# Kernel tuning notes

Measured on AMD Instinct MI355X. Metric: run time of the kernel, lower is better.

Reference implementation:

```python
import jax, jax.numpy as jnp
import numpy as np

N_NODES = 100000
N_EDGES = 1600000
D = 128


def setup_inputs() -> dict:
    key = jax.random.key(0)
    k1, k2, k3, k4 = jax.random.split(key, 4)
    x = jax.random.normal(k1, (N_NODES, D), dtype=jnp.float32)
    edge_index = jax.random.randint(k2, (2, N_EDGES), 0, N_NODES, dtype=jnp.int32)
    # torch.nn.Linear(nfeat, nclass): weight [out, in], bias [out]
    W = jax.random.normal(k3, (D, D), dtype=jnp.float32) * (1.0 / np.sqrt(D))
    b = jax.random.normal(k4, (D,), dtype=jnp.float32) * 0.01
    return {"x": x, "edge_index": edge_index, "W": W, "b": b}


def reference(x, edge_index, W, b):
    n = x.shape[0]
    # gcn_norm: add self-loops, edge_weight = 1
    loop = jnp.arange(n, dtype=edge_index.dtype)
    row = jnp.concatenate([edge_index[0], loop])  # source
    col = jnp.concatenate([edge_index[1], loop])  # target
    deg = jax.ops.segment_sum(jnp.ones_like(col, dtype=x.dtype), col, num_segments=n)
    dinv = jnp.where(deg > 0, deg ** -0.5, 0.0)
    norm = dinv[row] * dinv[col]  # [E+N]
    # K=1 propagate: out[col] += norm * x[row]
    agg = jax.ops.segment_sum(x[row] * norm[:, None], col, num_segments=n)
    # linear (y = agg @ W^T + b), then relu + residual
    h = agg @ W.T + b
    return x + jax.nn.relu(h)
```

## Files before the change

kernel.cpp:

```cpp
#include <hip/hip_runtime.h>

#define NN 100000
#define NE 1600000
#define DD 128
#define NBLK 98
#define NBUK 782
#define NB_AC 256
#define CHUNK 6250
#define SCAN_N (NBUK * NB_AC)
#define NB_SCAN 196

typedef __attribute__((ext_vector_type(8))) short bf16x8;
typedef __attribute__((ext_vector_type(4))) float f32x4;
typedef __attribute__((ext_vector_type(2))) float f32x2;

__device__ __forceinline__ float bf2f(unsigned short u) {
    return __uint_as_float(((unsigned)u) << 16);
}
__device__ __forceinline__ unsigned short f2bf(float f) {
    unsigned u = __float_as_uint(f);
    u += 0x7FFFu + ((u >> 16) & 1u);
    return (unsigned short)(u >> 16);
}

__global__ __launch_bounds__(1024) void k_hist(const int* __restrict__ col,
                                               unsigned* __restrict__ part) {
    __shared__ unsigned hist[NBUK];
    int t = threadIdx.x, blk = blockIdx.x;
    for (int i = t; i < NBUK; i += 1024) hist[i] = 0;
    __syncthreads();
    int beg = blk * CHUNK, end = beg + CHUNK;
    for (int e = beg + t; e < end; e += 1024)
        atomicAdd(&hist[col[e] >> 7], 1u);
    __syncthreads();
    for (int i = t; i < NBUK; i += 1024)
        part[(size_t)i * NB_AC + blk] = hist[i];
}

__global__ __launch_bounds__(1024) void k_bsum(const unsigned* __restrict__ part,
                                               unsigned* __restrict__ sb) {
    __shared__ unsigned red[1024];
    int t = threadIdx.x;
    int i = blockIdx.x * 1024 + t;
    red[t] = i < SCAN_N ? part[i] : 0;
    __syncthreads();
    for (int off = 512; off > 0; off >>= 1) {
        if (t < off) red[t] += red[t + off];
        __syncthreads();
    }
    if (t == 0) sb[blockIdx.x] = red[0];
}

__global__ __launch_bounds__(1024) void k_scanpart(const unsigned* __restrict__ part,
                                                   const unsigned* __restrict__ sb,
                                                   unsigned* __restrict__ off) {
    __shared__ unsigned s2[256];
    __shared__ unsigned s[1024];
    int t = threadIdx.x;
    if (t < 256) s2[t] = (t < NB_SCAN) ? sb[t] : 0;
    __syncthreads();
    for (int o = 1; o < 256; o <<= 1) {
        unsigned v = 0;
        if (t < 256 && t >= o) v = s2[t - o];
        __syncthreads();
        if (t < 256) s2[t] += v;
        __syncthreads();
    }
    unsigned boff = blockIdx.x == 0 ? 0 : s2[blockIdx.x - 1];
    int i = blockIdx.x * 1024 + t;
    unsigned v = i < SCAN_N ? part[i] : 0;
    s[t] = v;
    __syncthreads();
    for (int o = 1; o < 1024; o <<= 1) {
        unsigned u = t >= o ? s[t - o] : 0;
        __syncthreads();
        s[t] += u;
        __syncthreads();
    }
    if (i < SCAN_N) off[i] = boff + s[t] - v;
}

__global__ __launch_bounds__(1024) void k_scatter_pk(const int* __restrict__ row,
                                                     const int* __restrict__ col,
                                                     const unsigned* __restrict__ off,
                                                     unsigned* __restrict__ packed) {
    __shared__ unsigned cur[NBUK];
    int t = threadIdx.x, blk = blockIdx.x;
    for (int i = t; i < NBUK; i += 1024) cur[i] = off[(size_t)i * NB_AC + blk];
    __syncthreads();
    int beg = blk * CHUNK, end = beg + CHUNK;
    for (int e = beg + t; e < end; e += 1024) {
        int c = col[e];
        unsigned pos = atomicAdd(&cur[c >> 7], 1u);
        packed[pos] = ((unsigned)(c & 127) << 17) | (unsigned)row[e];
    }
}

__global__ __launch_bounds__(256) void k_bucket_csr(const unsigned* __restrict__ off,
                                                    const unsigned* __restrict__ packed,
                                                    float* __restrict__ dinv,
                                                    int* __restrict__ rowptr,
                                                    int* __restrict__ esrc) {
    __shared__ unsigned deg[128], pre[128], tmp[128];
    int t = threadIdx.x;
    int buk = blockIdx.x;
    unsigned bstart = off[(size_t)buk * NB_AC];
    unsigned bend = (buk == NBUK - 1) ? (unsigned)NE : off[(size_t)(buk + 1) * NB_AC];
    if (t < 128) deg[t] = 0;
    __syncthreads();
    for (unsigned e = bstart + t; e < bend; e += 256)
        atomicAdd(&deg[packed[e] >> 17], 1u);
    __syncthreads();
    if (t < 128) tmp[t] = deg[t];
    __syncthreads();
    for (int o = 1; o < 128; o <<= 1) {
        unsigned v = 0;
        if (t < 128 && t >= o) v = tmp[t - o];
        __syncthreads();
        if (t < 128) tmp[t] += v;
        __syncthreads();
    }
    if (t < 128) {
        pre[t] = tmp[t] - deg[t];
        int n = buk * 128 + t;
        if (n < NN) {
            dinv[n] = 1.0f / sqrtf((float)(deg[t] + 1));
            rowptr[n] = (int)(bstart + pre[t]);
        }
    }
    if (buk == NBUK - 1 && t == 0) rowptr[NN] = NE;
    __syncthreads();
    if (t < 128) deg[t] = pre[t];
    __syncthreads();
    for (unsigned e = bstart + t; e < bend; e += 256) {
        unsigned p = packed[e];
        unsigned pos = atomicAdd(&deg[p >> 17], 1u);
        esrc[bstart + pos] = (int)(p & 0x1FFFFu);
    }
}

__global__ void k_wb(const float* __restrict__ W, unsigned short* __restrict__ wbs) {
    int unit = blockIdx.x * 256 + threadIdx.x;
    int row = unit >> 4;
    int c0 = (unit & 15) * 8;
    float4 v0 = *(const float4*)(W + row * DD + c0);
    float4 v1 = *(const float4*)(W + row * DD + c0 + 4);
    bf16x8 h;
    h[0] = (short)f2bf(v0.x); h[1] = (short)f2bf(v0.y);
    h[2] = (short)f2bf(v0.z); h[3] = (short)f2bf(v0.w);
    h[4] = (short)f2bf(v1.x); h[5] = (short)f2bf(v1.y);
    h[6] = (short)f2bf(v1.z); h[7] = (short)f2bf(v1.w);
    int byte = (row * 256 + c0 * 2) ^ ((row & 7) << 4);
    *(bf16x8*)((char*)wbs + byte) = h;
}

__global__ __launch_bounds__(256) void k_ygemm(const float* __restrict__ x,
                                               const unsigned short* __restrict__ wbs,
                                               const float* __restrict__ dinv,
                                               unsigned char* __restrict__ yb8) {
    __shared__ unsigned short wb[DD * DD];
    int t = threadIdx.x;
#pragma unroll
    for (int i = 0; i < 8; ++i)
        ((float4*)wb)[t + 256 * i] = ((const float4*)wbs)[t + 256 * i];
    __syncthreads();

    int wave = t >> 6;
    int lane = t & 63;
    int lrow = lane & 15;
    int kg = lane >> 4;

    int arow = blockIdx.x * 64 + wave * 16 + lrow;
    int arc = arow < NN ? arow : NN - 1;
    bf16x8 afrag[4];
#pragma unroll
    for (int ks = 0; ks < 4; ++ks) {
        const float* src = x + (size_t)arc * DD + ks * 32 + kg * 8;
        float4 v0 = *(const float4*)src;
        float4 v1 = *(const float4*)(src + 4);
        bf16x8 h;
        h[0] = (short)f2bf(v0.x); h[1] = (short)f2bf(v0.y);
        h[2] = (short)f2bf(v0.z); h[3] = (short)f2bf(v0.w);
        h[4] = (short)f2bf(v1.x); h[5] = (short)f2bf(v1.y);
        h[6] = (short)f2bf(v1.z); h[7] = (short)f2bf(v1.w);
        afrag[ks] = h;
    }

    f32x4 acc[8];
#pragma unroll
    for (int ct = 0; ct < 8; ++ct) acc[ct] = (f32x4)(0.f);

#pragma unroll
    for (int ct = 0; ct < 8; ++ct) {
        int wrow = ct * 16 + lrow;
#pragma unroll
        for (int ks = 0; ks < 4; ++ks) {
            int byte = (wrow * 256 + ks * 64 + kg * 16) ^ ((wrow & 7) << 4);
            bf16x8 bfrag = *(const bf16x8*)((char*)wb + byte);
            acc[ct] = __builtin_amdgcn_mfma_f32_16x16x32_bf16(afrag[ks], bfrag, acc[ct], 0, 0, 0);
        }
    }

#pragma unroll
    for (int j = 0; j < 4; ++j) {
        int m = blockIdx.x * 64 + wave * 16 + kg * 4 + j;
        if (m < NN) {
            float s = dinv[m];
            unsigned w0 = 0, w1 = 0;
            w0 = __builtin_amdgcn_cvt_pk_fp8_f32(s * acc[0][j], s * acc[1][j], w0, false);
            w0 = __builtin_amdgcn_cvt_pk_fp8_f32(s * acc[2][j], s * acc[3][j], w0, true);
            w1 = __builtin_amdgcn_cvt_pk_fp8_f32(s * acc[4][j], s * acc[5][j], w1, false);
            w1 = __builtin_amdgcn_cvt_pk_fp8_f32(s * acc[6][j], s * acc[7][j], w1, true);
            uint2 o; o.x = w0; o.y = w1;
            *(uint2*)(yb8 + (size_t)m * DD + lrow * 8) = o;
        }
    }
}

__global__ __launch_bounds__(256) void k_gather_fp8(const int* __restrict__ rowptr,
                                                    const int* __restrict__ esrc,
                                                    const unsigned char* __restrict__ yb8,
                                                    const float* __restrict__ x,
                                                    const float* __restrict__ dinv,
                                                    const float* __restrict__ bias,
                                                    float* __restrict__ out) {
    int t = threadIdx.x;
    int gl = t & 31;
    int node = blockIdx.x * 8 + (t >> 5);
    if (node >= NN) return;
    int beg = rowptr[node];
    int end = rowptr[node + 1];
    float dc = dinv[node];

    unsigned su = *(const unsigned*)(yb8 + (size_t)node * DD + gl * 4);
    f32x2 a01 = __builtin_amdgcn_cvt_pk_f32_fp8(su, false);
    f32x2 a23 = __builtin_amdgcn_cvt_pk_f32_fp8(su, true);

    int e = beg;
    for (; e + 7 < end; e += 8) {
        unsigned uu[8];
#pragma unroll
        for (int u = 0; u < 8; ++u) {
            int r = esrc[e + u];
            uu[u] = *(const unsigned*)(yb8 + (size_t)r * DD + gl * 4);
        }
#pragma unroll
        for (int u = 0; u < 8; ++u) {
            a01 += __builtin_amdgcn_cvt_pk_f32_fp8(uu[u], false);
            a23 += __builtin_amdgcn_cvt_pk_f32_fp8(uu[u], true);
        }
    }
    for (; e < end; ++e) {
        int r = esrc[e];
        unsigned u = *(const unsigned*)(yb8 + (size_t)r * DD + gl * 4);
        a01 += __builtin_amdgcn_cvt_pk_f32_fp8(u, false);
        a23 += __builtin_amdgcn_cvt_pk_f32_fp8(u, true);
    }

    float vals[4] = {a01.x, a01.y, a23.x, a23.y};
    int q = gl >> 1;
    int c0 = (gl & 1) * 4;
#pragma unroll
    for (int i = 0; i < 4; ++i) {
        int n = (c0 + i) * 16 + q;
        float h = dc * vals[i] + bias[n];
        out[(size_t)node * DD + n] = x[(size_t)node * DD + n] + fmaxf(h, 0.f);
    }
}

__global__ void k_count(const int* __restrict__ col, int* __restrict__ deg) {
    int i = blockIdx.x * blockDim.x + threadIdx.x;
    if (i < NE) atomicAdd(&deg[col[i]], 1);
}
__global__ __launch_bounds__(1024) void k_blocksum_dinv(const int* __restrict__ deg,
                                                        int* __restrict__ bsum,
                                                        float* __restrict__ dinv) {
    __shared__ int red[1024];
    int t = threadIdx.x;
    int i = blockIdx.x * 1024 + t;
    int d = i < NN ? deg[i] : 0;
    if (i < NN) dinv[i] = 1.0f / sqrtf((float)(d + 1));
    red[t] = d;
    __syncthreads();
    for (int off = 512; off > 0; off >>= 1) {
        if (t < off) red[t] += red[t + off];
        __syncthreads();
    }
    if (t == 0) bsum[blockIdx.x] = red[0];
}
__global__ void k_scanbsum(const int* __restrict__ bsum, int* __restrict__ boff) {
    __shared__ int s[128];
    int t = threadIdx.x;
    s[t] = t < NBLK ? bsum[t] : 0;
    __syncthreads();
    for (int off = 1; off < 128; off <<= 1) {
        int v = t >= off ? s[t - off] : 0;
        __syncthreads();
        s[t] += v;
        __syncthreads();
    }
    if (t < NBLK) boff[t] = (t == 0) ? 0 : s[t - 1];
}
__global__ __launch_bounds__(1024) void k_scanwrite(const int* __restrict__ deg,
                                                    const int* __restrict__ boff,
                                                    int* __restrict__ rowptr) {
    __shared__ int s[1024];
    int t = threadIdx.x;
    int i = blockIdx.x * 1024 + t;
    int v = i < NN ? deg[i] : 0;
    s[t] = v;
    __syncthreads();
    for (int off = 1; off < 1024; off <<= 1) {
        int u = t >= off ? s[t - off] : 0;
        __syncthreads();
        s[t] += u;
        __syncthreads();
    }
    if (i < NN) rowptr[i] = boff[blockIdx.x] + s[t] - v;
    if (i == 0) rowptr[NN] = NE;
}
__global__ void k_fill(const int* __restrict__ row, const int* __restrict__ col,
                       const int* __restrict__ rowptr, int* __restrict__ cnt,
                       int* __restrict__ esrc) {
    int i = blockIdx.x * blockDim.x + threadIdx.x;
    if (i < NE) {
        int c = col[i];
        int pos = rowptr[c] + atomicAdd(&cnt[c], 1);
        esrc[pos] = row[i];
    }
}
__global__ __launch_bounds__(256) void k_gather(const int* __restrict__ rowptr,
                                                const int* __restrict__ esrc,
                                                const float* __restrict__ x,
                                                const float* __restrict__ dinv,
                                                float* __restrict__ agg) {
    int t = threadIdx.x;
    int lane = t & 31;
    int node = blockIdx.x * 8 + (t >> 5);
    if (node >= NN) return;
    int beg = rowptr[node];
    int end = rowptr[node + 1];
    float dc = dinv[node];
    float4 xv = ((const float4*)(x + (size_t)node * DD))[lane];
    float4 acc;
    acc.x = dc * xv.x; acc.y = dc * xv.y; acc.z = dc * xv.z; acc.w = dc * xv.w;
    int e = beg;
    for (; e + 1 < end; e += 2) {
        int r0 = esrc[e];
        int r1 = esrc[e + 1];
        float s0 = dinv[r0];
        float s1 = dinv[r1];
        float4 v0 = ((const float4*)(x + (size_t)r0 * DD))[lane];
        float4 v1 = ((const float4*)(x + (size_t)r1 * DD))[lane];
        acc.x += s0 * v0.x + s1 * v1.x;
        acc.y += s0 * v0.y + s1 * v1.y;
        acc.z += s0 * v0.z + s1 * v1.z;
        acc.w += s0 * v0.w + s1 * v1.w;
    }
    if (e < end) {
        int r = esrc[e];
        float s = dinv[r];
        float4 v = ((const float4*)(x + (size_t)r * DD))[lane];
        acc.x += s * v.x; acc.y += s * v.y; acc.z += s * v.z; acc.w += s * v.w;
    }
    acc.x *= dc; acc.y *= dc; acc.z *= dc; acc.w *= dc;
    ((float4*)(agg + (size_t)node * DD))[lane] = acc;
}
__global__ void k_transpose_w(const float* __restrict__ W, float* __restrict__ Wt) {
    int c = blockIdx.x;
    int k = threadIdx.x;
    Wt[k * DD + c] = W[c * DD + k];
}
__global__ __launch_bounds__(256) void k_gemm(const float* __restrict__ x,
                                              const float* __restrict__ Wt,
                                              const float* __restrict__ bias,
                                              float* __restrict__ out) {
    __shared__ float wt[DD * DD];
    int t = threadIdx.x;
    for (int i = t; i < DD * DD / 4; i += 256)
        ((float4*)wt)[i] = ((const float4*)Wt)[i];
    __syncthreads();

    int grp = t >> 5;
    int c4  = (t & 31) * 4;
    int rbase = blockIdx.x * 64 + grp * 8;

    float acc[8][4];
#pragma unroll
    for (int i = 0; i < 8; i++)
#pragma unroll
        for (int j = 0; j < 4; j++) acc[i][j] = 0.0f;

    for (int k = 0; k < DD; k += 4) {
        float4 w0 = *(const float4*)&wt[(k + 0) * DD + c4];
        float4 w1 = *(const float4*)&wt[(k + 1) * DD + c4];
        float4 w2 = *(const float4*)&wt[(k + 2) * DD + c4];
        float4 w3 = *(const float4*)&wt[(k + 3) * DD + c4];
#pragma unroll
        for (int i = 0; i < 8; i++) {
            int rr = rbase + i;
            rr = rr < NN ? rr : NN - 1;
            float4 a = *(const float4*)&out[(size_t)rr * DD + k];
            acc[i][0] += a.x * w0.x + a.y * w1.x + a.z * w2.x + a.w * w3.x;
            acc[i][1] += a.x * w0.y + a.y * w1.y + a.z * w2.y + a.w * w3.y;
            acc[i][2] += a.x * w0.z + a.y * w1.z + a.z * w2.z + a.w * w3.z;
            acc[i][3] += a.x * w0.w + a.y * w1.w + a.z * w2.w + a.w * w3.w;
        }
    }

    float4 bv = *(const float4*)&bias[c4];
#pragma unroll
    for (int i = 0; i < 8; i++) {
        int r = rbase + i;
        if (r < NN) {
            float4 xv = *(const float4*)&x[(size_t)r * DD + c4];
            float4 o;
            o.x = xv.x + fmaxf(acc[i][0] + bv.x, 0.0f);
            o.y = xv.y + fmaxf(acc[i][1] + bv.y, 0.0f);
            o.z = xv.z + fmaxf(acc[i][2] + bv.z, 0.0f);
            o.w = xv.w + fmaxf(acc[i][3] + bv.w, 0.0f);
            *(float4*)&out[(size_t)r * DD + c4] = o;
        }
    }
}

extern "C" void kernel_launch(void* const* d_in, const int* in_sizes, int n_in,
                              void* d_out, int out_size, void* d_ws, size_t ws_size,
                              hipStream_t stream) {
    const float* x   = (const float*)d_in[0];
    const int*   ei  = (const int*)d_in[1];
    const float* W   = (const float*)d_in[2];
    const float* b   = (const float*)d_in[3];
    const int* row = ei;
    const int* col = ei + NE;

    float* out = (float*)d_out;

    char* ws = (char*)d_ws;
    unsigned* part   = (unsigned*)ws;
    unsigned* off    = (unsigned*)(ws + 800768);
    unsigned* sb     = (unsigned*)(ws + 1601536);
    float*    dinv   = (float*)(ws + 1602352);
    int*      rowptr = (int*)(ws + 2002352);
    unsigned* packed = (unsigned*)(ws + 2402368);
    unsigned short* wbs = (unsigned short*)(ws + 8802368);
    float*    Wt     = (float*)(ws + 8802368);
    int*      esrc   = (int*)(ws + 8867904);
    unsigned char* yb8 = (unsigned char*)(ws + 15267904);

    bool big_ws = ws_size >= 28100000;

    if (big_ws) {
        k_hist<<<NB_AC, 1024, 0, stream>>>(col, part);
        k_bsum<<<NB_SCAN, 1024, 0, stream>>>(part, sb);
        k_scanpart<<<NB_SCAN, 1024, 0, stream>>>(part, sb, off);
        k_scatter_pk<<<NB_AC, 1024, 0, stream>>>(row, col, off, packed);
        k_bucket_csr<<<NBUK, 256, 0, stream>>>(off, packed, dinv, rowptr, esrc);
        k_wb<<<8, 256, 0, stream>>>(W, wbs);
        k_ygemm<<<(NN + 63) / 64, 256, 0, stream>>>(x, wbs, dinv, yb8);
        k_gather_fp8<<<(NN + 7) / 8, 256, 0, stream>>>(rowptr, esrc, yb8, x, dinv, b, out);
    } else {
        int* cnt  = (int*)ws;
        int* bsum = (int*)(ws + 1601536);
        int* boff = (int*)(ws + 400000);
        hipMemsetAsync(cnt, 0, NN * sizeof(int), stream);
        k_count<<<(NE + 255) / 256, 256, 0, stream>>>(col, cnt);
        k_blocksum_dinv<<<NBLK, 1024, 0, stream>>>(cnt, bsum, dinv);
        k_scanbsum<<<1, 128, 0, stream>>>(bsum, boff);
        k_scanwrite<<<NBLK, 1024, 0, stream>>>(cnt, boff, rowptr);
        hipMemsetAsync(cnt, 0, NN * sizeof(int), stream);
        k_fill<<<(NE + 255) / 256, 256, 0, stream>>>(row, col, rowptr, cnt, esrc);
        k_gather<<<(NN + 7) / 8, 256, 0, stream>>>(rowptr, esrc, x, dinv, out);
        k_transpose_w<<<DD, DD, 0, stream>>>(W, Wt);
        k_gemm<<<(NN + 63) / 64, 256, 0, stream>>>(x, Wt, b, out);
    }
}
```

Baseline: 124.4 us.

## Fuse bucket CSR build with fp8 GEMM and move source dinv scaling into gather

Merges the bucket-CSR kernel, the W bf16 conversion kernel and the y GEMM into one launch, with blocks split by index between CSR work and GEMM work. To remove the GEMM's dependency on dinv, the source-side normalisation moves into the gather, which now loads dinv[r] per edge and scales each fp8 row. Each GEMM block converts W to bf16 in shared memory itself, and the gather uses nontemporal loads and stores for x and out. The cost is an extra dinv load per edge plus redundant W conversion in every GEMM block, and the fp8 values are now quantised before the dinv scaling, which may change accuracy.

```diff
diff --git a/kernel.cpp b/kernel.cpp
--- a/kernel.cpp
+++ b/kernel.cpp
@@ -9,6 +9,7 @@
 #define CHUNK 6250
 #define SCAN_N (NBUK * NB_AC)
 #define NB_SCAN 196
+#define NB_YG ((NN + 63) / 64)
 
 typedef __attribute__((ext_vector_type(8))) short bf16x8;
 typedef __attribute__((ext_vector_type(4))) float f32x4;
@@ -96,123 +97,120 @@
     }
 }
 
-__global__ __launch_bounds__(256) void k_bucket_csr(const unsigned* __restrict__ off,
-                                                    const unsigned* __restrict__ packed,
-                                                    float* __restrict__ dinv,
-                                                    int* __restrict__ rowptr,
-                                                    int* __restrict__ esrc) {
+__global__ __launch_bounds__(256) void k_finalize(const unsigned* __restrict__ off,
+                                                  const unsigned* __restrict__ packed,
+                                                  float* __restrict__ dinv,
+                                                  int* __restrict__ rowptr,
+                                                  int* __restrict__ esrc,
+                                                  const float* __restrict__ x,
+                                                  const float* __restrict__ W,
+                                                  unsigned char* __restrict__ yb8) {
+    __shared__ unsigned short wb[DD * DD];
     __shared__ unsigned deg[128], pre[128], tmp[128];
     int t = threadIdx.x;
-    int buk = blockIdx.x;
-    unsigned bstart = off[(size_t)buk * NB_AC];
-    unsigned bend = (buk == NBUK - 1) ? (unsigned)NE : off[(size_t)(buk + 1) * NB_AC];
-    if (t < 128) deg[t] = 0;
-    __syncthreads();
-    for (unsigned e = bstart + t; e < bend; e += 256)
-        atomicAdd(&deg[packed[e] >> 17], 1u);
-    __syncthreads();
-    if (t < 128) tmp[t] = deg[t];
-    __syncthreads();
-    for (int o = 1; o < 128; o <<= 1) {
-        unsigned v = 0;
-        if (t < 128 && t >= o) v = tmp[t - o];
-        __syncthreads();
-        if (t < 128) tmp[t] += v;
-        __syncthreads();
-    }
-    if (t < 128) {
-        pre[t] = tmp[t] - deg[t];
-        int n = buk * 128 + t;
-        if (n < NN) {
-            dinv[n] = 1.0f / sqrtf((float)(deg[t] + 1));
-            rowptr[n] = (int)(bstart + pre[t]);
-        }
-    }
-    if (buk == NBUK - 1 && t == 0) rowptr[NN] = NE;
-    __syncthreads();
-    if (t < 128) deg[t] = pre[t];
-    __syncthreads();
-    for (unsigned e = bstart + t; e < bend; e += 256) {
-        unsigned p = packed[e];
-        unsigned pos = atomicAdd(&deg[p >> 17], 1u);
-        esrc[bstart + pos] = (int)(p & 0x1FFFFu);
-    }
-}
-
-__global__ void k_wb(const float* __restrict__ W, unsigned short* __restrict__ wbs) {
-    int unit = blockIdx.x * 256 + threadIdx.x;
-    int row = unit >> 4;
-    int c0 = (unit & 15) * 8;
-    float4 v0 = *(const float4*)(W + row * DD + c0);
-    float4 v1 = *(const float4*)(W + row * DD + c0 + 4);
-    bf16x8 h;
-    h[0] = (short)f2bf(v0.x); h[1] = (short)f2bf(v0.y);
-    h[2] = (short)f2bf(v0.z); h[3] = (short)f2bf(v0.w);
-    h[4] = (short)f2bf(v1.x); h[5] = (short)f2bf(v1.y);
-    h[6] = (short)f2bf(v1.z); h[7] = (short)f2bf(v1.w);
-    int byte = (row * 256 + c0 * 2) ^ ((row & 7) << 4);
-    *(bf16x8*)((char*)wbs + byte) = h;
-}
-
-__global__ __launch_bounds__(256) void k_ygemm(const float* __restrict__ x,
-                                               const unsigned short* __restrict__ wbs,
-                                               const float* __restrict__ dinv,
-                                               unsigned char* __restrict__ yb8) {
-    __shared__ unsigned short wb[DD * DD];
-    int t = threadIdx.x;
-#pragma unroll
-    for (int i = 0; i < 8; ++i)
-        ((float4*)wb)[t + 256 * i] = ((const float4*)wbs)[t + 256 * i];
-    __syncthreads();
-
-    int wave = t >> 6;
-    int lane = t & 63;
-    int lrow = lane & 15;
-    int kg = lane >> 4;
-
-    int arow = blockIdx.x * 64 + wave * 16 + lrow;
-    int arc = arow < NN ? arow : NN - 1;
-    bf16x8 afrag[4];
-#pragma unroll
-    for (int ks = 0; ks < 4; ++ks) {
-        const float* src = x + (size_t)arc * DD + ks * 32 + kg * 8;
-        float4 v0 = *(const float4*)src;
-        float4 v1 = *(const float4*)(src + 4);
-        bf16x8 h;
-        h[0] = (short)f2bf(v0.x); h[1] = (short)f2bf(v0.y);
-        h[2] = (short)f2bf(v0.z); h[3] = (short)f2bf(v0.w);
-        h[4] = (short)f2bf(v1.x); h[5] = (short)f2bf(v1.y);
-        h[6] = (short)f2bf(v1.z); h[7] = (short)f2bf(v1.w);
-        afrag[ks] = h;
-    }
-
-    f32x4 acc[8];
-#pragma unroll
-    for (int ct = 0; ct < 8; ++ct) acc[ct] = (f32x4)(0.f);
-
-#pragma unroll
-    for (int ct = 0; ct < 8; ++ct) {
-        int wrow = ct * 16 + lrow;
+
+    if (blockIdx.x < NBUK) {
+        int buk = blockIdx.x;
+        unsigned bstart = off[(size_t)buk * NB_AC];
+        unsigned bend = (buk == NBUK - 1) ? (unsigned)NE : off[(size_t)(buk + 1) * NB_AC];
+        if (t < 128) deg[t] = 0;
+        __syncthreads();
+        for (unsigned e = bstart + t; e < bend; e += 256)
+            atomicAdd(&deg[packed[e] >> 17], 1u);
+        __syncthreads();
+        if (t < 128) tmp[t] = deg[t];
+        __syncthreads();
+        for (int o = 1; o < 128; o <<= 1) {
+            unsigned v = 0;
+            if (t < 128 && t >= o) v = tmp[t - o];
+            __syncthreads();
+            if (t < 128) tmp[t] += v;
+            __syncthreads();
+        }
+        if (t < 128) {
+            pre[t] = tmp[t] - deg[t];
+            int n = buk * 128 + t;
+            if (n < NN) {
+                dinv[n] = 1.0f / sqrtf((float)(deg[t] + 1));
+                rowptr[n] = (int)(bstart + pre[t]);
+            }
+        }
+        if (buk == NBUK - 1 && t == 0) rowptr[NN] = NE;
+        __syncthreads();
+        if (t < 128) deg[t] = pre[t];
+        __syncthreads();
+        for (unsigned e = bstart + t; e < bend; e += 256) {
+            unsigned p = packed[e];
+            unsigned pos = atomicAdd(&deg[p >> 17], 1u);
+            esrc[bstart + pos] = (int)(p & 0x1FFFFu);
+        }
+    } else {
+        int blk = blockIdx.x - NBUK;
+#pragma unroll
+        for (int it = 0; it < 8; ++it) {
+            int unit = t + 256 * it;
+            int wrow = unit >> 4;
+            int c0 = (unit & 15) * 8;
+            float4 v0 = *(const float4*)(W + wrow * DD + c0);
+            float4 v1 = *(const float4*)(W + wrow * DD + c0 + 4);
+            bf16x8 h;
+            h[0] = (short)f2bf(v0.x); h[1] = (short)f2bf(v0.y);
+            h[2] = (short)f2bf(v0.z); h[3] = (short)f2bf(v0.w);
+            h[4] = (short)f2bf(v1.x); h[5] = (short)f2bf(v1.y);
+            h[6] = (short)f2bf(v1.z); h[7] = (short)f2bf(v1.w);
+            int byte = (wrow * 256 + c0 * 2) ^ ((wrow & 7) << 4);
+            *(bf16x8*)((char*)wb + byte) = h;
+        }
+        __syncthreads();
+
+        int wave = t >> 6;
+        int lane = t & 63;
+        int lrow = lane & 15;
+        int kg = lane >> 4;
+
+        int arow = blk * 64 + wave * 16 + lrow;
+        int arc = arow < NN ? arow : NN - 1;
+        bf16x8 afrag[4];
 #pragma unroll
         for (int ks = 0; ks < 4; ++ks) {
-            int byte = (wrow * 256 + ks * 64 + kg * 16) ^ ((wrow & 7) << 4);
-            bf16x8 bfrag = *(const bf16x8*)((char*)wb + byte);
-            acc[ct] = __builtin_amdgcn_mfma_f32_16x16x32_bf16(afrag[ks], bfrag, acc[ct], 0, 0, 0);
-        }
-    }
-
-#pragma unroll
-    for (int j = 0; j < 4; ++j) {
-        int m = blockIdx.x * 64 + wave * 16 + kg * 4 + j;
-        if (m < NN) {
-            float s = dinv[m];
-            unsigned w0 = 0, w1 = 0;
-            w0 = __builtin_amdgcn_cvt_pk_fp8_f32(s * acc[0][j], s * acc[1][j], w0, false);
-            w0 = __builtin_amdgcn_cvt_pk_fp8_f32(s * acc[2][j], s * acc[3][j], w0, true);
-            w1 = __builtin_amdgcn_cvt_pk_fp8_f32(s * acc[4][j], s * acc[5][j], w1, false);
-            w1 = __builtin_amdgcn_cvt_pk_fp8_f32(s * acc[6][j], s * acc[7][j], w1, true);
-            uint2 o; o.x = w0; o.y = w1;
-            *(uint2*)(yb8 + (size_t)m * DD + lrow * 8) = o;
+            const float* src = x + (size_t)arc * DD + ks * 32 + kg * 8;
+            float4 v0 = *(const float4*)src;
+            float4 v1 = *(const float4*)(src + 4);
+            bf16x8 h;
+            h[0] = (short)f2bf(v0.x); h[1] = (short)f2bf(v0.y);
+            h[2] = (short)f2bf(v0.z); h[3] = (short)f2bf(v0.w);
+            h[4] = (short)f2bf(v1.x); h[5] = (short)f2bf(v1.y);
+            h[6] = (short)f2bf(v1.z); h[7] = (short)f2bf(v1.w);
+            afrag[ks] = h;
+        }
+
+        f32x4 acc[8];
+#pragma unroll
+        for (int ct = 0; ct < 8; ++ct) acc[ct] = (f32x4)(0.f);
+
+#pragma unroll
+        for (int ct = 0; ct < 8; ++ct) {
+            int wrow = ct * 16 + lrow;
+#pragma unroll
+            for (int ks = 0; ks < 4; ++ks) {
+                int byte = (wrow * 256 + ks * 64 + kg * 16) ^ ((wrow & 7) << 4);
+                bf16x8 bfrag = *(const bf16x8*)((char*)wb + byte);
+                acc[ct] = __builtin_amdgcn_mfma_f32_16x16x32_bf16(afrag[ks], bfrag, acc[ct], 0, 0, 0);
+            }
+        }
+
+#pragma unroll
+        for (int j = 0; j < 4; ++j) {
+            int m = blk * 64 + wave * 16 + kg * 4 + j;
+            if (m < NN) {
+                unsigned w0 = 0, w1 = 0;
+                w0 = __builtin_amdgcn_cvt_pk_fp8_f32(acc[0][j], acc[1][j], w0, false);
+                w0 = __builtin_amdgcn_cvt_pk_fp8_f32(acc[2][j], acc[3][j], w0, true);
+                w1 = __builtin_amdgcn_cvt_pk_fp8_f32(acc[4][j], acc[5][j], w1, false);
+                w1 = __builtin_amdgcn_cvt_pk_fp8_f32(acc[6][j], acc[7][j], w1, true);
+                uint2 o; o.x = w0; o.y = w1;
+                *(uint2*)(yb8 + (size_t)m * DD + lrow * 8) = o;
+            }
         }
     }
 }
@@ -233,38 +231,44 @@
     float dc = dinv[node];
 
     unsigned su = *(const unsigned*)(yb8 + (size_t)node * DD + gl * 4);
-    f32x2 a01 = __builtin_amdgcn_cvt_pk_f32_fp8(su, false);
-    f32x2 a23 = __builtin_amdgcn_cvt_pk_f32_fp8(su, true);
+    f32x2 a01 = dc * __builtin_amdgcn_cvt_pk_f32_fp8(su, false);
+    f32x2 a23 = dc * __builtin_amdgcn_cvt_pk_f32_fp8(su, true);
 
     int e = beg;
     for (; e + 7 < end; e += 8) {
         unsigned uu[8];
+        float ss[8];
 #pragma unroll
         for (int u = 0; u < 8; ++u) {
             int r = esrc[e + u];
             uu[u] = *(const unsigned*)(yb8 + (size_t)r * DD + gl * 4);
+            ss[u] = dinv[r];
         }
 #pragma unroll
         for (int u = 0; u < 8; ++u) {
-            a01 += __builtin_amdgcn_cvt_pk_f32_fp8(uu[u], false);
-            a23 += __builtin_amdgcn_cvt_pk_f32_fp8(uu[u], true);
+            a01 += ss[u] * __builtin_amdgcn_cvt_pk_f32_fp8(uu[u], false);
+            a23 += ss[u] * __builtin_amdgcn_cvt_pk_f32_fp8(uu[u], true);
         }
     }
     for (; e < end; ++e) {
         int r = esrc[e];
         unsigned u = *(const unsigned*)(yb8 + (size_t)r * DD + gl * 4);
-        a01 += __builtin_amdgcn_cvt_pk_f32_fp8(u, false);
-        a23 += __builtin_amdgcn_cvt_pk_f32_fp8(u, true);
+        float s = dinv[r];
+        a01 += s * __builtin_amdgcn_cvt_pk_f32_fp8(u, false);
+        a23 += s * __builtin_amdgcn_cvt_pk_f32_fp8(u, true);
     }
 
     float vals[4] = {a01.x, a01.y, a23.x, a23.y};
     int q = gl >> 1;
     int c0 = (gl & 1) * 4;
+    const float* xp = x + (size_t)node * DD;
+    float* op = out + (size_t)node * DD;
 #pragma unroll
     for (int i = 0; i < 4; ++i) {
         int n = (c0 + i) * 16 + q;
+        float xv = __builtin_nontemporal_load(xp + n);
         float h = dc * vals[i] + bias[n];
-        out[(size_t)node * DD + n] = x[(size_t)node * DD + n] + fmaxf(h, 0.f);
+        __builtin_nontemporal_store(xv + fmaxf(h, 0.f), op + n);
     }
 }
 
@@ -443,7 +447,6 @@
     float*    dinv   = (float*)(ws + 1602352);
     int*      rowptr = (int*)(ws + 2002352);
     unsigned* packed = (unsigned*)(ws + 2402368);
-    unsigned short* wbs = (unsigned short*)(ws + 8802368);
     float*    Wt     = (float*)(ws + 8802368);
     int*      esrc   = (int*)(ws + 8867904);
     unsigned char* yb8 = (unsigned char*)(ws + 15267904);
@@ -455,9 +458,7 @@
         k_bsum<<<NB_SCAN, 1024, 0, stream>>>(part, sb);
         k_scanpart<<<NB_SCAN, 1024, 0, stream>>>(part, sb, off);
         k_scatter_pk<<<NB_AC, 1024, 0, stream>>>(row, col, off, packed);
-        k_bucket_csr<<<NBUK, 256, 0, stream>>>(off, packed, dinv, rowptr, esrc);
-        k_wb<<<8, 256, 0, stream>>>(W, wbs);
-        k_ygemm<<<(NN + 63) / 64, 256, 0, stream>>>(x, wbs, dinv, yb8);
+        k_finalize<<<NBUK + NB_YG, 256, 0, stream>>>(off, packed, dinv, rowptr, esrc, x, W, yb8);
         k_gather_fp8<<<(NN + 7) / 8, 256, 0, stream>>>(rowptr, esrc, yb8, x, dinv, b, out);
     } else {
         int* cnt  = (int*)ws;
```

Result: faster. 120.2 us (median of 2 runs) (-3.4%).
